# Kernel tuning notes

Hardware: AMD Instinct MI355X
Metric: run time of the kernel (lower is better)

## Reference

```python
import jax, jax.numpy as jnp
import numpy as np

NUM_CLASSES = 21
IOU_THRESH = 0.5
NEG_POS_RATIO = 3
VAR0, VAR1 = 0.1, 0.2


def point_form(priors):
    # (cx,cy,w,h) -> (xmin,ymin,xmax,ymax)
    return jnp.concatenate([priors[:, :2] - priors[:, 2:] / 2,
                            priors[:, :2] + priors[:, 2:] / 2], axis=-1)


def jaccard(box_a, box_b):
    # box_a: [n,4] point form, box_b: [N,4] point form -> [n,N]
    max_xy = jnp.minimum(box_a[:, None, 2:], box_b[None, :, 2:])
    min_xy = jnp.maximum(box_a[:, None, :2], box_b[None, :, :2])
    inter = jnp.prod(jnp.clip(max_xy - min_xy, 0.0, None), axis=-1)
    area_a = jnp.prod(box_a[:, 2:] - box_a[:, :2], axis=-1)[:, None]
    area_b = jnp.prod(box_b[:, 2:] - box_b[:, :2], axis=-1)[None, :]
    return inter / (area_a + area_b - inter)


def encode(matched, priors):
    # matched: [N,4] point form, priors: [N,4] center form
    g_cxcy = ((matched[:, :2] + matched[:, 2:]) / 2 - priors[:, :2]) / (VAR0 * priors[:, 2:])
    g_wh = jnp.log((matched[:, 2:] - matched[:, :2]) / priors[:, 2:]) / VAR1
    return jnp.concatenate([g_cxcy, g_wh], axis=-1)


def match_one(truths, labels, priors):
    # truths: [n_obj,4], labels: [n_obj], priors: [N,4] center form
    ov = jaccard(truths, point_form(priors))          # [n_obj, N]
    best_prior_idx = jnp.argmax(ov, axis=1)           # [n_obj]
    best_truth_overlap = jnp.max(ov, axis=0)          # [N]
    best_truth_idx = jnp.argmax(ov, axis=0)           # [N]
    best_truth_overlap = best_truth_overlap.at[best_prior_idx].set(2.0)
    def body(j, bti):
        return bti.at[best_prior_idx[j]].set(j)
    best_truth_idx = jax.lax.fori_loop(0, truths.shape[0], body, best_truth_idx)
    matched = truths[best_truth_idx]                  # [N,4]
    conf = labels[best_truth_idx].astype(jnp.int32) + 1
    conf = jnp.where(best_truth_overlap < IOU_THRESH, 0, conf)
    return encode(matched, priors), conf


def smooth_l1(x):
    ax = jnp.abs(x)
    return jnp.where(ax < 1.0, 0.5 * x * x, ax - 0.5)


def setup_inputs() -> dict:
    key = jax.random.key(0)
    k1, k2, k3, k4, k5, k6, k7 = jax.random.split(key, 7)
    B, N, n_obj = 128, 8732, 16
    loc_data = jax.random.normal(k1, (B, N, 4), jnp.float32)
    conf_data = jax.random.normal(k2, (B, N, NUM_CLASSES), jnp.float32)
    # valid ground-truth boxes in [0,1], point form, plus class label in [0,20)
    mins = jax.random.uniform(k3, (B, n_obj, 2)) * 0.6
    sizes = jax.random.uniform(k4, (B, n_obj, 2)) * 0.35 + 0.05
    labels = jax.random.randint(k5, (B, n_obj), 0, NUM_CLASSES - 1).astype(jnp.float32)
    targets = jnp.concatenate([mins, mins + sizes, labels[..., None]], axis=-1)
    # priors in center form with positive w,h
    centers = jax.random.uniform(k6, (N, 2))
    wh = jax.random.uniform(k7, (N, 2)) * 0.5 + 0.05
    priors = jnp.concatenate([centers, wh], axis=-1).astype(jnp.float32)
    return {"loc_data": loc_data, "conf_data": conf_data, "targets": targets, "priors": priors}


def _forward(loc_data, conf_data, targets, priors):
    B, N = loc_data.shape[0], loc_data.shape[1]
    truths, labels = targets[:, :, :4], targets[:, :, 4]
    target_loc, target_conf = jax.vmap(match_one, in_axes=(0, 0, None))(truths, labels, priors)
    pos = target_conf > 0                             # [B,N]
    # localization: smooth-L1 summed over positive priors
    loss_l = jnp.sum(smooth_l1(loc_data - target_loc) * pos[..., None].astype(loc_data.dtype))
    # per-prior CE surrogate: logsumexp - logit[target]
    lse = jax.nn.logsumexp(conf_data, axis=-1)        # [B,N]
    gathered = jnp.take_along_axis(conf_data, target_conf[..., None], axis=-1)[..., 0]
    loss_c_all = lse - gathered                       # [B,N]
    # hard negative mining via double argsort ranking (positives excluded)
    lc = jnp.where(pos, 0.0, loss_c_all)
    loss_idx = jnp.argsort(-lc, axis=1)
    idx_rank = jnp.argsort(loss_idx, axis=1)
    num_pos = jnp.sum(pos.astype(jnp.int32), axis=1, keepdims=True)   # [B,1]
    num_neg = jnp.minimum(NEG_POS_RATIO * num_pos, N - 1)
    neg = idx_rank < num_neg
    sel = pos | neg
    loss_c = jnp.sum(jnp.where(sel, loss_c_all, 0.0))
    n_total = jnp.sum(num_pos).astype(loc_data.dtype)
    return loss_l / n_total, loss_c / n_total


def reference(loc_data, conf_data, targets, priors):
    return _forward(loc_data, conf_data, targets, priors)
```

## Files before the change

### kernel.cpp

```cpp
#include <hip/hip_runtime.h>
#include <cstdint>
#include <cstddef>

#define HB1 4096
#define HB2 2048
#define CMAX 21
#define IOU_T 0.5f

__device__ __forceinline__ float sl1(float x) {
    float ax = fabsf(x);
    return ax < 1.0f ? 0.5f * x * x : ax - 0.5f;
}

__global__ __launch_bounds__(256) void kA_best_prior(
    const float* __restrict__ targets, const float* __restrict__ priors,
    float* __restrict__ bpi_val, int* __restrict__ bpi_idx,
    int* __restrict__ num_pos_g, float* __restrict__ accB_g,
    float* __restrict__ acc_g, unsigned* __restrict__ done_g,
    int N, int NOBJ, int SLICES, int CHUNK, int B)
{
    const int s = blockIdx.x, b = blockIdx.y, t = threadIdx.x;
    __shared__ float tb[16 * 4];
    __shared__ float ta[16];
    __shared__ float wv[4 * 16];
    __shared__ int   wi[4 * 16];

    if (s == 0 && b == 0) {
        for (int q = t; q < B; q += 256) num_pos_g[q] = 0;
        for (int q = t; q < 2 * B; q += 256) accB_g[q] = 0.f;
        if (t < 4) acc_g[t] = 0.f;
        if (t == 0) *done_g = 0u;
    }

    if (t < 16) {
        if (t < NOBJ) {
            const float* tr = targets + ((size_t)b * NOBJ + t) * 5;
            float x0 = tr[0], y0 = tr[1], x1 = tr[2], y1 = tr[3];
            tb[t * 4 + 0] = x0; tb[t * 4 + 1] = y0;
            tb[t * 4 + 2] = x1; tb[t * 4 + 3] = y1;
            ta[t] = (x1 - x0) * (y1 - y0);
        } else {
            tb[t * 4 + 0] = 0.f; tb[t * 4 + 1] = 0.f;
            tb[t * 4 + 2] = 0.f; tb[t * 4 + 3] = 0.f;
            ta[t] = 0.f;
        }
    }
    __syncthreads();

    float bv[16]; int bi[16];
#pragma unroll
    for (int j = 0; j < 16; j++) { bv[j] = -1.0f; bi[j] = 0x7fffffff; }

    const int start = s * CHUNK;
    const int end = min(start + CHUNK, N);
    for (int i = start + t; i < end; i += 256) {
        float4 p = ((const float4*)priors)[i];
        float bx0 = p.x - p.z * 0.5f, by0 = p.y - p.w * 0.5f;
        float bx1 = p.x + p.z * 0.5f, by1 = p.y + p.w * 0.5f;
        float ab = (bx1 - bx0) * (by1 - by0);
#pragma unroll
        for (int j = 0; j < 16; j++) {
            float iw = fminf(tb[j * 4 + 2], bx1) - fmaxf(tb[j * 4 + 0], bx0);
            float ih = fminf(tb[j * 4 + 3], by1) - fmaxf(tb[j * 4 + 1], by0);
            iw = fmaxf(iw, 0.f); ih = fmaxf(ih, 0.f);
            float inter = iw * ih;
            float iou = inter / (ta[j] + ab - inter);
            if (iou > bv[j] || (iou == bv[j] && i < bi[j])) { bv[j] = iou; bi[j] = i; }
        }
    }

#pragma unroll
    for (int off = 32; off >= 1; off >>= 1) {
#pragma unroll
        for (int j = 0; j < 16; j++) {
            float v2 = __shfl_down(bv[j], off, 64);
            int   i2 = __shfl_down(bi[j], off, 64);
            if (v2 > bv[j] || (v2 == bv[j] && i2 < bi[j])) { bv[j] = v2; bi[j] = i2; }
        }
    }
    const int wid = t >> 6, lane = t & 63;
    if (lane == 0) {
#pragma unroll
        for (int j = 0; j < 16; j++) { wv[wid * 16 + j] = bv[j]; wi[wid * 16 + j] = bi[j]; }
    }
    __syncthreads();
    if (t < 16) {
        float v = wv[t]; int idx = wi[t];
#pragma unroll
        for (int w = 1; w < 4; w++) {
            float v2 = wv[w * 16 + t]; int i2 = wi[w * 16 + t];
            if (v2 > v || (v2 == v && i2 < idx)) { v = v2; idx = i2; }
        }
        if (t < NOBJ) {
            int o = (b * SLICES + s) * 16 + t;
            bpi_val[o] = v;
            bpi_idx[o] = idx;
        }
    }
}

#define IOU_STEP(j) { \
    float4 tj = tb4[j]; \
    float taj = (tj.z - tj.x) * (tj.w - tj.y); \
    float iw = fminf(tj.z, bx1) - fmaxf(tj.x, bx0); \
    float ih = fminf(tj.w, by1) - fmaxf(tj.y, by0); \
    iw = fmaxf(iw, 0.f); ih = fmaxf(ih, 0.f); \
    float inter = iw * ih; \
    float iou = inter * __builtin_amdgcn_rcpf(taj + ab - inter); \
    if (iou > bto) { bto = iou; bti = (j); } }

__global__ __launch_bounds__(256, 3) void kB_main(
    const float* __restrict__ loc, const float* __restrict__ conf,
    const float* __restrict__ targets, const float* __restrict__ priors,
    const float* __restrict__ bpi_val, const int* __restrict__ bpi_idx,
    float* __restrict__ lc_out, int* __restrict__ num_pos, float* __restrict__ accB,
    int N, int NOBJ, int SLICES, int TPB, int BPB)
{
    const int g = blockIdx.x;
    const int b = g / BPB;
    const int j0 = g % BPB;
    const int t = threadIdx.x;
    const int wid = t >> 6, lane = t & 63;

    __shared__ __align__(16) float buf[2][256 * CMAX];
    __shared__ __align__(16) float tb[16 * 4];
    __shared__ float tl[16];
    __shared__ __align__(16) int bpi_s[16];
    __shared__ float wred[4 * 3];

    if (t < 16) {
        if (t < NOBJ) {
            const float* tr = targets + ((size_t)b * NOBJ + t) * 5;
            tb[t * 4 + 0] = tr[0]; tb[t * 4 + 1] = tr[1];
            tb[t * 4 + 2] = tr[2]; tb[t * 4 + 3] = tr[3];
            tl[t] = tr[4];
            float bv = -1.f; int bi = 0x7fffffff;
            for (int s2 = 0; s2 < SLICES; s2++) {
                int o = (b * SLICES + s2) * 16 + t;
                float v = bpi_val[o]; int idx = bpi_idx[o];
                if (v > bv || (v == bv && idx < bi)) { bv = v; bi = idx; }
            }
            bpi_s[t] = bi;
        } else {
            tb[t * 4 + 0] = 0.f; tb[t * 4 + 1] = 0.f; tb[t * 4 + 2] = 0.f; tb[t * 4 + 3] = 0.f;
            tl[t] = 0.f; bpi_s[t] = -1;
        }
    }

    const float* confB = conf + (size_t)b * N * CMAX;
    const float* locB  = loc + (size_t)b * N * 4;

    float4 r0, r1, r2, r3, r4, r5, pld, ppr;

    auto stage = [&](int xx) {
        int i0s = xx * 256;
        int rows_s = min(256, N - i0s);
        int nf4s = (rows_s * CMAX) >> 2;
        const float4* s4 = (const float4*)(confB + (size_t)i0s * CMAX);
        if (t + 0    < nf4s) r0 = s4[t + 0];
        if (t + 256  < nf4s) r1 = s4[t + 256];
        if (t + 512  < nf4s) r2 = s4[t + 512];
        if (t + 768  < nf4s) r3 = s4[t + 768];
        if (t + 1024 < nf4s) r4 = s4[t + 1024];
        if (t + 1280 < nf4s) r5 = s4[t + 1280];
        if (t < rows_s) {
            ppr = ((const float4*)priors)[i0s + t];
            pld = ((const float4*)locB)[i0s + t];
        }
    };

    float ll = 0.f, plc = 0.f, np = 0.f;
    int x = j0, p = 0;
    if (x < TPB) stage(x);

    while (x < TPB) {
        const int i0 = x * 256;
        const int rows = min(256, N - i0);
        const int nf4 = (rows * CMAX) >> 2;

        float4 myp = ppr, myl = pld;

        float4* bp4f = (float4*)buf[p];
        if (t + 0    < nf4) bp4f[t + 0]    = r0;
        if (t + 256  < nf4) bp4f[t + 256]  = r1;
        if (t + 512  < nf4) bp4f[t + 512]  = r2;
        if (t + 768  < nf4) bp4f[t + 768]  = r3;
        if (t + 1024 < nf4) bp4f[t + 1024] = r4;
        if (t + 1280 < nf4) bp4f[t + 1280] = r5;
        __syncthreads();

        int xn = x + BPB;
        if (xn < TPB) stage(xn);

        if (t < rows) {
            const int i = i0 + t;
            float4 pp = myp;
            float bx0 = pp.x - pp.z * 0.5f, by0 = pp.y - pp.w * 0.5f;
            float bx1 = pp.x + pp.z * 0.5f, by1 = pp.y + pp.w * 0.5f;
            float ab = (bx1 - bx0) * (by1 - by0);
            float bto = -1.f; int bti = 0;
            const float4* tb4 = (const float4*)tb;
            if (NOBJ == 16) {
#pragma unroll
                for (int j = 0; j < 16; j++) IOU_STEP(j);
            } else {
                for (int j = 0; j < NOBJ; j++) IOU_STEP(j);
            }
            const int4* bp4 = (const int4*)bpi_s;
#pragma unroll
            for (int jj = 0; jj < 4; jj++) {
                int4 q = bp4[jj];
                if (q.x == i) { bto = 2.0f; bti = jj * 4 + 0; }
                if (q.y == i) { bto = 2.0f; bti = jj * 4 + 1; }
                if (q.z == i) { bto = 2.0f; bti = jj * 4 + 2; }
                if (q.w == i) { bto = 2.0f; bti = jj * 4 + 3; }
            }
            bool pos = !(bto < IOU_T);
            if (pos) {
                float4 tj = tb4[bti];
                float rz = __builtin_amdgcn_rcpf(pp.z);
                float rw = __builtin_amdgcn_rcpf(pp.w);
                float gcx = ((tj.x + tj.z) * 0.5f - pp.x) * (10.0f * rz);
                float gcy = ((tj.y + tj.w) * 0.5f - pp.y) * (10.0f * rw);
                float gw = __logf((tj.z - tj.x) * rz) * 5.0f;
                float gh = __logf((tj.w - tj.y) * rw) * 5.0f;
                ll += sl1(myl.x - gcx) + sl1(myl.y - gcy) + sl1(myl.z - gw) + sl1(myl.w - gh);
                np += 1.f;
            }
            int cf = pos ? ((int)tl[bti] + 1) : 0;
            const float* cr = buf[p] + t * CMAX;
            float m = cr[0];
#pragma unroll
            for (int c = 1; c < CMAX; c++) m = fmaxf(m, cr[c]);
            float ssum = 0.f;
#pragma unroll
            for (int c = 0; c < CMAX; c++) ssum += __expf(cr[c] - m);
            float lse = m + __logf(ssum);
            float lossc = lse - cr[cf];
            if (pos) plc += lossc;
            float lcv = pos ? 0.f : lossc;
            lcv = fmaxf(lcv, 0.f);
            lc_out[(size_t)b * N + i] = lcv;
        }
        p ^= 1;
        x = xn;
    }

#pragma unroll
    for (int off = 32; off >= 1; off >>= 1) {
        ll  += __shfl_down(ll, off, 64);
        plc += __shfl_down(plc, off, 64);
        np  += __shfl_down(np, off, 64);
    }
    if (lane == 0) { wred[wid * 3 + 0] = ll; wred[wid * 3 + 1] = plc; wred[wid * 3 + 2] = np; }
    __syncthreads();
    if (t == 0) {
        float a0 = 0.f, a1 = 0.f, a2 = 0.f;
#pragma unroll
        for (int w = 0; w < 4; w++) { a0 += wred[w * 3 + 0]; a1 += wred[w * 3 + 1]; a2 += wred[w * 3 + 2]; }
        atomicAdd(&accB[b * 2 + 0], a0);
        atomicAdd(&accB[b * 2 + 1], a1);
        atomicAdd(&num_pos[b], (int)a2);
    }
}

__device__ __forceinline__ void wave_sufscan(int& c, float& s, int lane) {
#pragma unroll
    for (int off = 1; off < 64; off <<= 1) {
        int c2 = __shfl_down(c, off, 64);
        float s2 = __shfl_down(s, off, 64);
        if (lane + off < 64) { c += c2; s += s2; }
    }
}

__global__ __launch_bounds__(1024) void kC_topk(
    const float* __restrict__ lc, const int* __restrict__ num_pos,
    const float* __restrict__ accB,
    float* __restrict__ acc, unsigned* __restrict__ done_ctr,
    float* __restrict__ out, int N, int B)
{
    const int b = blockIdx.x, t = threadIdx.x;
    const int NT = 1024;
    const int wid = t >> 6, lane = t & 63;
    __shared__ __align__(16) int   cnt[HB1];
    __shared__ __align__(16) float sm[HB1];
    __shared__ int   wc[16];
    __shared__ float ws[16];
    __shared__ int s_strad, s_krem;
    __shared__ float s_above;
    __shared__ int s_last;
    __shared__ float wsum[16], wsA[16], wsB[16];

    const int k = min(3 * num_pos[b], N - 1);
    const float* lcb = lc + (size_t)b * N;
    float total = 0.f;

    if (k > 0) {
        ((int4*)cnt)[t] = make_int4(0, 0, 0, 0);
        ((float4*)sm)[t] = make_float4(0.f, 0.f, 0.f, 0.f);
        __syncthreads();
        const int n4 = N >> 2;
        const float4* lcb4 = (const float4*)lcb;
        for (int i = t; i < n4; i += NT) {
            float4 v = lcb4[i];
            { unsigned u = __float_as_uint(v.x) >> 19; atomicAdd(&cnt[u], 1); atomicAdd(&sm[u], v.x); }
            { unsigned u = __float_as_uint(v.y) >> 19; atomicAdd(&cnt[u], 1); atomicAdd(&sm[u], v.y); }
            { unsigned u = __float_as_uint(v.z) >> 19; atomicAdd(&cnt[u], 1); atomicAdd(&sm[u], v.z); }
            { unsigned u = __float_as_uint(v.w) >> 19; atomicAdd(&cnt[u], 1); atomicAdd(&sm[u], v.w); }
        }
        for (int i = (n4 << 2) + t; i < N; i += NT) {
            float v = lcb[i];
            unsigned u = __float_as_uint(v) >> 19;
            atomicAdd(&cnt[u], 1); atomicAdd(&sm[u], v);
        }
        __syncthreads();
        {
            int4  cv = ((const int4*)cnt)[t];
            float4 sv = ((const float4*)sm)[t];
            int   ci = cv.x + cv.y + cv.z + cv.w;
            float si = sv.x + sv.y + sv.z + sv.w;
            wave_sufscan(ci, si, lane);
            if (lane == 0) { wc[wid] = ci; ws[wid] = si; }
            __syncthreads();
            int cab = 0; float sab = 0.f;
            for (int w = wid + 1; w < 16; w++) { cab += wc[w]; sab += ws[w]; }
            int   i0c = ci + cab;          float f0 = si + sab;
            int   i1c = i0c - cv.x;        float f1 = f0 - sv.x;
            int   i2c = i1c - cv.y;        float f2 = f1 - sv.y;
            int   i3c = i2c - cv.z;        float f3 = f2 - sv.z;
            int   i4c = i3c - cv.w;
            if (i1c < k && k <= i0c) { s_strad = 4 * t + 0; s_krem = k - i1c; s_above = f1; }
            if (i2c < k && k <= i1c) { s_strad = 4 * t + 1; s_krem = k - i2c; s_above = f2; }
            if (i3c < k && k <= i2c) { s_strad = 4 * t + 2; s_krem = k - i3c; s_above = f3; }
            if (i4c < k && k <= i3c) { s_strad = 4 * t + 3; s_krem = k - i4c; s_above = f3 - sv.w; }
        }
        __syncthreads();
        const int s1 = s_strad, k2 = s_krem;
        total += s_above;

        __syncthreads();
        ((int2*)cnt)[t] = make_int2(0, 0);
        ((float2*)sm)[t] = make_float2(0.f, 0.f);
        __syncthreads();
        for (int i = t; i < N; i += NT) {
            float v = lcb[i];
            unsigned u = __float_as_uint(v);
            if ((int)(u >> 19) == s1) {
                int q = (int)((u >> 8) & 0x7FF);
                atomicAdd(&cnt[q], 1); atomicAdd(&sm[q], v);
            }
        }
        __syncthreads();
        {
            int2  cv = ((const int2*)cnt)[t];
            float2 sv = ((const float2*)sm)[t];
            int   ci = cv.x + cv.y;
            float si = sv.x + sv.y;
            wave_sufscan(ci, si, lane);
            if (lane == 0) { wc[wid] = ci; ws[wid] = si; }
            __syncthreads();
            int cab = 0; float sab = 0.f;
            for (int w = wid + 1; w < 16; w++) { cab += wc[w]; sab += ws[w]; }
            int   i0c = ci + cab;       float f0 = si + sab;
            int   i1c = i0c - cv.x;     float f1 = f0 - sv.x;
            int   i2c = i1c - cv.y;
            if (i1c < k2 && k2 <= i0c) { s_strad = 2 * t + 0; s_krem = k2 - i1c; s_above = f1; }
            if (i2c < k2 && k2 <= i1c) { s_strad = 2 * t + 1; s_krem = k2 - i2c; s_above = f1 - sv.y; }
        }
        __syncthreads();
        const int s2 = s_strad, krem = s_krem;
        total += s_above;
        float tval = __uint_as_float((((unsigned)s1) << 19) | (((unsigned)s2) << 8));
        total += (float)krem * tval;
    }

    if (t == 0) {
        if (k > 0) atomicAdd(&acc[1], total);
        __threadfence();
        unsigned old = atomicAdd(done_ctr, 1u);
        s_last = (old == (unsigned)gridDim.x - 1u) ? 1 : 0;
    }
    __syncthreads();
    if (s_last) {
        __threadfence();
        float vn = 0.f, va = 0.f, vb = 0.f;
        for (int q = t; q < B; q += NT) {
            vn += (float)num_pos[q];
            va += accB[q * 2 + 0];
            vb += accB[q * 2 + 1];
        }
#pragma unroll
        for (int off = 32; off >= 1; off >>= 1) {
            vn += __shfl_down(vn, off, 64);
            va += __shfl_down(va, off, 64);
            vb += __shfl_down(vb, off, 64);
        }
        if (lane == 0) { wsum[wid] = vn; wsA[wid] = va; wsB[wid] = vb; }
        __syncthreads();
        if (t == 0) {
            float n = 0.f, a = 0.f, bsum = 0.f;
#pragma unroll
            for (int w = 0; w < 16; w++) { n += wsum[w]; a += wsA[w]; bsum += wsB[w]; }
            float l2 = atomicAdd(&acc[1], 0.0f);
            out[0] = a / n;
            out[1] = (bsum + l2) / n;
        }
    }
}

extern "C" void kernel_launch(void* const* d_in, const int* in_sizes, int n_in,
                              void* d_out, int out_size, void* d_ws, size_t ws_size,
                              hipStream_t stream)
{
    const float* loc     = (const float*)d_in[0];
    const float* conf    = (const float*)d_in[1];
    const float* targets = (const float*)d_in[2];
    const float* priors  = (const float*)d_in[3];
    float* out = (float*)d_out;

    const int N = in_sizes[3] / 4;
    const int BN = in_sizes[0] / 4;
    const int B = BN / N;
    const int NOBJ = in_sizes[2] / (B * 5);
    const int SLICES = 8;
    const int CHUNK = (N + SLICES - 1) / SLICES;
    const int TPB = (N + 255) / 256;
    const int BPB = 6;

    char* w = (char*)d_ws;
    float*    lc_ws   = (float*)w;                         size_t off = (size_t)BN * 4;
    float*    bpi_val = (float*)(w + off);                 off += (size_t)B * SLICES * 16 * 4;
    int*      bpi_idx = (int*)(w + off);                   off += (size_t)B * SLICES * 16 * 4;
    int*      num_pos = (int*)(w + off);                   off += (size_t)B * 4;
    float*    accB    = (float*)(w + off);                 off += (size_t)B * 2 * 4;
    float*    acc     = (float*)(w + off);                 off += 16;
    unsigned* done    = (unsigned*)(w + off);              off += 16;

    dim3 gA(SLICES, B);
    kA_best_prior<<<gA, 256, 0, stream>>>(targets, priors, bpi_val, bpi_idx,
                                          num_pos, accB, acc, done, N, NOBJ, SLICES, CHUNK, B);

    kB_main<<<B * BPB, 256, 0, stream>>>(loc, conf, targets, priors, bpi_val, bpi_idx,
                                         lc_ws, num_pos, accB, N, NOBJ, SLICES, TPB, BPB);

    kC_topk<<<B, 1024, 0, stream>>>(lc_ws, num_pos, accB, acc, done, out, N, B);
}
```

Measured before the change: 225.5 us.

## Replace LDS double-buffered conf staging with direct per-thread global loads

Removes the shared-memory double buffer that staged confidence rows with coalesced float4 loads. Each thread now loads its own 21 logits straight from global memory into registers, and the target-class logit is selected with a register select. Dropping the large LDS footprint allows more blocks per CU, raising the launch-bounds occupancy hint and the number of blocks per batch. The risk is less coalesced 84-byte-strided loads and the loss of explicit prefetch overlap.

```diff
diff --git a/kernel.cpp b/kernel.cpp
--- a/kernel.cpp
+++ b/kernel.cpp
@@ -109,12 +109,12 @@
     float iou = inter * __builtin_amdgcn_rcpf(taj + ab - inter); \
     if (iou > bto) { bto = iou; bti = (j); } }
 
-__global__ __launch_bounds__(256, 3) void kB_main(
+__global__ __launch_bounds__(256, 4) void kB_main(
     const float* __restrict__ loc, const float* __restrict__ conf,
     const float* __restrict__ targets, const float* __restrict__ priors,
     const float* __restrict__ bpi_val, const int* __restrict__ bpi_idx,
     float* __restrict__ lc_out, int* __restrict__ num_pos, float* __restrict__ accB,
-    int N, int NOBJ, int SLICES, int TPB, int BPB)
+    int N, int NOBJ, int SLICES, int BPB)
 {
     const int g = blockIdx.x;
     const int b = g / BPB;
@@ -122,7 +122,6 @@
     const int t = threadIdx.x;
     const int wid = t >> 6, lane = t & 63;
 
-    __shared__ __align__(16) float buf[2][256 * CMAX];
     __shared__ __align__(16) float tb[16 * 4];
     __shared__ float tl[16];
     __shared__ __align__(16) int bpi_s[16];
@@ -146,104 +145,71 @@
             tl[t] = 0.f; bpi_s[t] = -1;
         }
     }
+    __syncthreads();
 
     const float* confB = conf + (size_t)b * N * CMAX;
     const float* locB  = loc + (size_t)b * N * 4;
 
-    float4 r0, r1, r2, r3, r4, r5, pld, ppr;
-
-    auto stage = [&](int xx) {
-        int i0s = xx * 256;
-        int rows_s = min(256, N - i0s);
-        int nf4s = (rows_s * CMAX) >> 2;
-        const float4* s4 = (const float4*)(confB + (size_t)i0s * CMAX);
-        if (t + 0    < nf4s) r0 = s4[t + 0];
-        if (t + 256  < nf4s) r1 = s4[t + 256];
-        if (t + 512  < nf4s) r2 = s4[t + 512];
-        if (t + 768  < nf4s) r3 = s4[t + 768];
-        if (t + 1024 < nf4s) r4 = s4[t + 1024];
-        if (t + 1280 < nf4s) r5 = s4[t + 1280];
-        if (t < rows_s) {
-            ppr = ((const float4*)priors)[i0s + t];
-            pld = ((const float4*)locB)[i0s + t];
-        }
-    };
-
     float ll = 0.f, plc = 0.f, np = 0.f;
-    int x = j0, p = 0;
-    if (x < TPB) stage(x);
-
-    while (x < TPB) {
-        const int i0 = x * 256;
-        const int rows = min(256, N - i0);
-        const int nf4 = (rows * CMAX) >> 2;
-
-        float4 myp = ppr, myl = pld;
-
-        float4* bp4f = (float4*)buf[p];
-        if (t + 0    < nf4) bp4f[t + 0]    = r0;
-        if (t + 256  < nf4) bp4f[t + 256]  = r1;
-        if (t + 512  < nf4) bp4f[t + 512]  = r2;
-        if (t + 768  < nf4) bp4f[t + 768]  = r3;
-        if (t + 1024 < nf4) bp4f[t + 1024] = r4;
-        if (t + 1280 < nf4) bp4f[t + 1280] = r5;
-        __syncthreads();
-
-        int xn = x + BPB;
-        if (xn < TPB) stage(xn);
-
-        if (t < rows) {
-            const int i = i0 + t;
-            float4 pp = myp;
-            float bx0 = pp.x - pp.z * 0.5f, by0 = pp.y - pp.w * 0.5f;
-            float bx1 = pp.x + pp.z * 0.5f, by1 = pp.y + pp.w * 0.5f;
-            float ab = (bx1 - bx0) * (by1 - by0);
-            float bto = -1.f; int bti = 0;
-            const float4* tb4 = (const float4*)tb;
-            if (NOBJ == 16) {
-#pragma unroll
-                for (int j = 0; j < 16; j++) IOU_STEP(j);
-            } else {
-                for (int j = 0; j < NOBJ; j++) IOU_STEP(j);
-            }
-            const int4* bp4 = (const int4*)bpi_s;
-#pragma unroll
-            for (int jj = 0; jj < 4; jj++) {
-                int4 q = bp4[jj];
-                if (q.x == i) { bto = 2.0f; bti = jj * 4 + 0; }
-                if (q.y == i) { bto = 2.0f; bti = jj * 4 + 1; }
-                if (q.z == i) { bto = 2.0f; bti = jj * 4 + 2; }
-                if (q.w == i) { bto = 2.0f; bti = jj * 4 + 3; }
-            }
-            bool pos = !(bto < IOU_T);
-            if (pos) {
-                float4 tj = tb4[bti];
-                float rz = __builtin_amdgcn_rcpf(pp.z);
-                float rw = __builtin_amdgcn_rcpf(pp.w);
-                float gcx = ((tj.x + tj.z) * 0.5f - pp.x) * (10.0f * rz);
-                float gcy = ((tj.y + tj.w) * 0.5f - pp.y) * (10.0f * rw);
-                float gw = __logf((tj.z - tj.x) * rz) * 5.0f;
-                float gh = __logf((tj.w - tj.y) * rw) * 5.0f;
-                ll += sl1(myl.x - gcx) + sl1(myl.y - gcy) + sl1(myl.z - gw) + sl1(myl.w - gh);
-                np += 1.f;
-            }
-            int cf = pos ? ((int)tl[bti] + 1) : 0;
-            const float* cr = buf[p] + t * CMAX;
-            float m = cr[0];
-#pragma unroll
-            for (int c = 1; c < CMAX; c++) m = fmaxf(m, cr[c]);
-            float ssum = 0.f;
-#pragma unroll
-            for (int c = 0; c < CMAX; c++) ssum += __expf(cr[c] - m);
-            float lse = m + __logf(ssum);
-            float lossc = lse - cr[cf];
-            if (pos) plc += lossc;
-            float lcv = pos ? 0.f : lossc;
-            lcv = fmaxf(lcv, 0.f);
-            lc_out[(size_t)b * N + i] = lcv;
-        }
-        p ^= 1;
-        x = xn;
+
+    const int stride = BPB * 256;
+    for (int i = j0 * 256 + t; i < N; i += stride) {
+        float4 pp  = ((const float4*)priors)[i];
+        float4 myl = ((const float4*)locB)[i];
+        const float* cr = confB + (size_t)i * CMAX;
+        float c[CMAX];
+#pragma unroll
+        for (int q = 0; q < CMAX; q++) c[q] = cr[q];
+
+        float bx0 = pp.x - pp.z * 0.5f, by0 = pp.y - pp.w * 0.5f;
+        float bx1 = pp.x + pp.z * 0.5f, by1 = pp.y + pp.w * 0.5f;
+        float ab = (bx1 - bx0) * (by1 - by0);
+        float bto = -1.f; int bti = 0;
+        const float4* tb4 = (const float4*)tb;
+        if (NOBJ == 16) {
+#pragma unroll
+            for (int j = 0; j < 16; j++) IOU_STEP(j);
+        } else {
+            for (int j = 0; j < NOBJ; j++) IOU_STEP(j);
+        }
+        const int4* bp4 = (const int4*)bpi_s;
+#pragma unroll
+        for (int jj = 0; jj < 4; jj++) {
+            int4 q = bp4[jj];
+            if (q.x == i) { bto = 2.0f; bti = jj * 4 + 0; }
+            if (q.y == i) { bto = 2.0f; bti = jj * 4 + 1; }
+            if (q.z == i) { bto = 2.0f; bti = jj * 4 + 2; }
+            if (q.w == i) { bto = 2.0f; bti = jj * 4 + 3; }
+        }
+        bool pos = !(bto < IOU_T);
+        if (pos) {
+            float4 tj = tb4[bti];
+            float rz = __builtin_amdgcn_rcpf(pp.z);
+            float rw = __builtin_amdgcn_rcpf(pp.w);
+            float gcx = ((tj.x + tj.z) * 0.5f - pp.x) * (10.0f * rz);
+            float gcy = ((tj.y + tj.w) * 0.5f - pp.y) * (10.0f * rw);
+            float gw = __logf((tj.z - tj.x) * rz) * 5.0f;
+            float gh = __logf((tj.w - tj.y) * rw) * 5.0f;
+            ll += sl1(myl.x - gcx) + sl1(myl.y - gcy) + sl1(myl.z - gw) + sl1(myl.w - gh);
+            np += 1.f;
+        }
+        int cf = pos ? ((int)tl[bti] + 1) : 0;
+
+        float m = c[0];
+#pragma unroll
+        for (int q = 1; q < CMAX; q++) m = fmaxf(m, c[q]);
+        float ssum = 0.f;
+#pragma unroll
+        for (int q = 0; q < CMAX; q++) ssum += __expf(c[q] - m);
+        float gath = c[0];
+#pragma unroll
+        for (int q = 1; q < CMAX; q++) gath = (q == cf) ? c[q] : gath;
+        float lse = m + __logf(ssum);
+        float lossc = lse - gath;
+        if (pos) plc += lossc;
+        float lcv = pos ? 0.f : lossc;
+        lcv = fmaxf(lcv, 0.f);
+        lc_out[(size_t)b * N + i] = lcv;
     }
 
 #pragma unroll
@@ -424,8 +390,7 @@
     const int NOBJ = in_sizes[2] / (B * 5);
     const int SLICES = 8;
     const int CHUNK = (N + SLICES - 1) / SLICES;
-    const int TPB = (N + 255) / 256;
-    const int BPB = 6;
+    const int BPB = 12;
 
     char* w = (char*)d_ws;
     float*    lc_ws   = (float*)w;                         size_t off = (size_t)BN * 4;
@@ -441,7 +406,7 @@
                                           num_pos, accB, acc, done, N, NOBJ, SLICES, CHUNK, B);
 
     kB_main<<<B * BPB, 256, 0, stream>>>(loc, conf, targets, priors, bpi_val, bpi_idx,
-                                         lc_ws, num_pos, accB, N, NOBJ, SLICES, TPB, BPB);
+                                         lc_ws, num_pos, accB, N, NOBJ, SLICES, BPB);
 
     kC_topk<<<B, 1024, 0, stream>>>(lc_ws, num_pos, accB, acc, done, out, N, B);
 }
```

New measurement: 269.2 us. 1.19x slower.
